# Optimization experiments

Hardware: AMD Instinct MI355X
Metric: run time of the kernel (lower is better)

Reference implementation:

```python
import jax, jax.numpy as jnp
import numpy as np
import math

B, S, D, H = 2, 2048, 1024, 16
HD = D // H  # head dim = 64


def _rope_tables():
    # RoFormer sinusoidal position embedding: one frequency per (even, odd) pair
    pos = jnp.arange(S, dtype=jnp.float32)[:, None]                # [S, 1]
    inv_freq = 1.0 / (10000.0 ** (jnp.arange(0, HD, 2, dtype=jnp.float32) / HD))  # [HD/2]
    ang = pos * inv_freq[None, :]                                   # [S, HD/2]
    sin = jnp.sin(ang)[None, None]                                  # [1,1,S,HD/2]
    cos = jnp.cos(ang)[None, None]
    return sin, cos


def setup_inputs() -> dict:
    key = jax.random.key(0)
    k0, k1, k2, k3 = jax.random.split(key, 4)
    scale = 1.0 / math.sqrt(D)
    sin, cos = _rope_tables()
    return {
        "hidden_states": jax.random.normal(k0, (B, S, D), dtype=jnp.float32),
        "Wq": jax.random.normal(k1, (D, D), dtype=jnp.float32) * scale,
        "Wk": jax.random.normal(k2, (D, D), dtype=jnp.float32) * scale,
        "Wv": jax.random.normal(k3, (D, D), dtype=jnp.float32) * scale,
        "sin": sin,
        "cos": cos,
    }


def _split_heads(x):
    # [B,S,D] -> [B,H,S,HD]
    b, s, _ = x.shape
    return x.reshape(b, s, H, HD).transpose(0, 2, 1, 3)


def _apply_rotary(x, sin, cos):
    # x: [B,H,S,HD]; sin/cos broadcast as [1,1,S,HD/2]
    x1 = x[..., 0::2]
    x2 = x[..., 1::2]
    out = jnp.stack([x1 * cos - x2 * sin, x2 * cos + x1 * sin], axis=-1)
    return out.reshape(x.shape)


def reference(hidden_states, Wq, Wk, Wv, sin, cos):
    q = _apply_rotary(_split_heads(hidden_states @ Wq), sin, cos)  # [B,H,S,HD]
    k = _apply_rotary(_split_heads(hidden_states @ Wk), sin, cos)
    v = _apply_rotary(_split_heads(hidden_states @ Wv), sin, cos)  # note: RoPE on V too, per source
    scores = jnp.einsum("bhqd,bhkd->bhqk", q, k) / math.sqrt(HD)   # [B,H,S,S]
    probs = jax.nn.softmax(scores, axis=-1)
    ctx = jnp.einsum("bhqk,bhkd->bhqd", probs, v)                   # [B,H,S,HD]
    return ctx.transpose(0, 2, 1, 3).reshape(hidden_states.shape[0], S, D)
```

## Files before the change

### kernel.cpp

```cpp
#include <hip/hip_runtime.h>

typedef unsigned short u16;
typedef unsigned short u16x8 __attribute__((ext_vector_type(8)));
typedef unsigned short u16x4 __attribute__((ext_vector_type(4)));
typedef __bf16 bf16x8_t __attribute__((ext_vector_type(8)));
typedef float floatx4 __attribute__((ext_vector_type(4)));

#define BATCH 2
#define S_LEN 2048
#define D_DIM 1024
#define NH    16
#define HD    64

__device__ __forceinline__ u16 f2b(float f) {
  union { float f; unsigned int i; } c; c.f = f;
  const unsigned int i = c.i;
  return (u16)((i + 0x7FFFu + ((i >> 16) & 1u)) >> 16);
}
__device__ __forceinline__ bf16x8_t asbf(u16x8 v) {
  union { u16x8 u; bf16x8_t b; } c; c.u = v; return c.b;
}
__device__ __forceinline__ void load_lds16(const u16* g, u16* l) {
  __builtin_amdgcn_global_load_lds(
      (const __attribute__((address_space(1))) void*)g,
      (__attribute__((address_space(3))) void*)l, 16, 0, 0);
}

__device__ __attribute__((aligned(256))) u16 g_xb[(size_t)BATCH * S_LEN * D_DIM];
__device__ __attribute__((aligned(256))) u16 g_wt[3u * D_DIM * D_DIM];
__device__ __attribute__((aligned(256))) u16 g_qkv[3u * BATCH * S_LEN * D_DIM];

__global__ __launch_bounds__(256) void convert_x(const float* __restrict__ X) {
  const size_t i = ((size_t)blockIdx.x * 256 + threadIdx.x) * 8;
  floatx4 a = *(const floatx4*)(X + i);
  floatx4 b = *(const floatx4*)(X + i + 4);
  u16x8 o;
#pragma unroll
  for (int j = 0; j < 4; ++j) { o[j] = f2b(a[j]); o[4 + j] = f2b(b[j]); }
  *(u16x8*)(g_xb + i) = o;
}

__global__ __launch_bounds__(256) void transpose_w(const float* __restrict__ W, int z) {
  __shared__ u16 t[64][65];
  u16* Wt = g_wt + (size_t)z * D_DIM * D_DIM;
  const int k0 = blockIdx.x * 64;
  const int n0 = blockIdx.y * 64;
  const int tid = threadIdx.x;
  const int rr = tid >> 4;
  const int cc = (tid & 15) * 4;
#pragma unroll
  for (int i = 0; i < 4; ++i) {
    const int r = rr + i * 16;
    floatx4 v = *(const floatx4*)(W + (size_t)(k0 + r) * D_DIM + n0 + cc);
    t[r][cc] = f2b(v[0]); t[r][cc + 1] = f2b(v[1]);
    t[r][cc + 2] = f2b(v[2]); t[r][cc + 3] = f2b(v[3]);
  }
  __syncthreads();
#pragma unroll
  for (int i = 0; i < 4; ++i) {
    const int r = rr + i * 16;
    u16x4 v;
    v[0] = t[cc][r]; v[1] = t[cc + 1][r]; v[2] = t[cc + 2][r]; v[3] = t[cc + 3][r];
    *(u16x4*)(Wt + (size_t)(n0 + r) * D_DIM + k0 + cc) = v;
  }
}

__global__ __launch_bounds__(256) void qkv_gemm(const float* __restrict__ sin_t,
                                                const float* __restrict__ cos_t) {
  __shared__ __attribute__((aligned(16))) u16 lds_a[128 * 32];
  __shared__ __attribute__((aligned(16))) u16 lds_b[128 * 32];
  const int tid = threadIdx.x;
  const int wv = tid >> 6;
  const int lane = tid & 63;
  const int lrow = lane & 15;
  const int quad = lane >> 4;
  const int wr = wv >> 1, wc = wv & 1;
  const int m0 = blockIdx.x * 128;
  const int n0 = blockIdx.y * 128;
  const int z = blockIdx.z;
  const bool vmode = (z == 2);
  const u16* Wz = g_wt + (size_t)z * (D_DIM * D_DIM);

  floatx4 acc[4][4] = {};

  const int srow = lane >> 2;
  const int scol = (lane & 3) * 8;
  const u16* gA = g_xb + (size_t)(m0 + wv * 32 + srow) * D_DIM + scol;
  const u16* gB = Wz   + (size_t)(n0 + wv * 32 + srow) * D_DIM + scol;
  u16* sA = &lds_a[(wv * 32) * 32];
  u16* sB = &lds_b[(wv * 32) * 32];

  const u16* Aarr = vmode ? lds_b : lds_a;
  const u16* Barr = vmode ? lds_a : lds_b;

  for (int k0 = 0; k0 < D_DIM; k0 += 32) {
    __syncthreads();
    load_lds16(gA + k0, sA);
    load_lds16(gA + (size_t)16 * D_DIM + k0, sA + 512);
    load_lds16(gB + k0, sB);
    load_lds16(gB + (size_t)16 * D_DIM + k0, sB + 512);
    __syncthreads();
    u16x8 af[4], bfr[4];
#pragma unroll
    for (int mi = 0; mi < 4; ++mi)
      af[mi] = *(const u16x8*)&Aarr[(wr * 64 + mi * 16 + lrow) * 32 + quad * 8];
#pragma unroll
    for (int ni = 0; ni < 4; ++ni)
      bfr[ni] = *(const u16x8*)&Barr[(wc * 64 + ni * 16 + lrow) * 32 + quad * 8];
#pragma unroll
    for (int mi = 0; mi < 4; ++mi)
#pragma unroll
      for (int ni = 0; ni < 4; ++ni)
        acc[mi][ni] = __builtin_amdgcn_mfma_f32_16x16x32_bf16(
            asbf(af[mi]), asbf(bfr[ni]), acc[mi][ni], 0, 0, 0);
  }

  if (!vmode) {
    u16* outz = g_qkv + (size_t)z * (BATCH * S_LEN * D_DIM);
#pragma unroll
    for (int mi = 0; mi < 4; ++mi) {
      const int m = m0 + wr * 64 + mi * 16 + quad * 4;
      const int b = m >> 11;
#pragma unroll
      for (int ni = 0; ni < 4; ++ni) {
        const int n = n0 + wc * 64 + ni * 16 + lrow;
        const int h = n >> 6, hd = n & 63;
        const int i0 = hd >> 1;
        const float sgn = (hd & 1) ? 1.f : -1.f;
        u16* op = outz + (((size_t)(b * NH + h) * S_LEN + (m & 2047)) * HD + hd);
#pragma unroll
        for (int r = 0; r < 4; ++r) {
          const int s = (m + r) & 2047;
          const float c  = cos_t[(size_t)s * 32 + i0];
          const float sn = sin_t[(size_t)s * 32 + i0];
          const float v = acc[mi][ni][r];
          const float vp = __shfl_xor(v, 1);
          op[r * HD] = f2b(v * c + sgn * sn * vp);
        }
      }
    }
  } else {
    u16* outv = g_qkv + (size_t)2 * (BATCH * S_LEN * D_DIM);
#pragma unroll
    for (int mi = 0; mi < 4; ++mi) {
      const int hb = n0 + wr * 64 + mi * 16 + quad * 4;
#pragma unroll
      for (int ni = 0; ni < 4; ++ni) {
        const int sg = m0 + wc * 64 + ni * 16 + lrow;
        const int b = sg >> 11, s = sg & 2047;
#pragma unroll
        for (int r = 0; r < 4; ++r) {
          const int hdg = hb + r;
          const int h = (hdg >> 6) & 15, hd = hdg & 63;
          const float c  = cos_t[(size_t)s * 32 + (hd >> 1)];
          const float sn = sin_t[(size_t)s * 32 + (hd >> 1)];
          const float v  = acc[mi][ni][r];
          const float vp = acc[mi][ni][r ^ 1];
          const float val = (r & 1) ? (v * c + sn * vp) : (v * c - sn * vp);
          outv[((size_t)(b * NH + h) * HD + hd) * S_LEN + s] = f2b(val);
        }
      }
    }
  }
}

__global__ __launch_bounds__(256) void flash_attn(float* __restrict__ out) {
  __shared__ __attribute__((aligned(16))) u16 lds_k[64 * 72];
  __shared__ __attribute__((aligned(16))) u16 lds_v[64 * 72];
  __shared__ __attribute__((aligned(16))) u16 lds_p[4][16 * 64];
  const int bh = blockIdx.x;
  const int qt = blockIdx.y;
  const int b = bh >> 4, h = bh & 15;
  const int tid = threadIdx.x, wv = tid >> 6, lane = tid & 63;
  const int lrow = lane & 15, quad = lane >> 4;
  const u16* Qb  = g_qkv + (size_t)bh * (S_LEN * HD);
  const u16* Kb  = g_qkv + (size_t)(BATCH * NH + bh) * (S_LEN * HD);
  const u16* VTb = g_qkv + (size_t)(2 * BATCH * NH + bh) * (S_LEN * HD);
  const int q0 = qt * 64 + wv * 16;

  u16x8 qf[2];
#pragma unroll
  for (int ks = 0; ks < 2; ++ks)
    qf[ks] = *(const u16x8*)(Qb + (size_t)(q0 + lrow) * HD + ks * 32 + quad * 8);

  floatx4 oacc[4] = {};
  float l_part[4] = {0.f, 0.f, 0.f, 0.f};
  const float cexp = 0.125f * 1.44269504088896f;

  const int sr = tid >> 3;
  const int sc = (tid & 7) * 8;
  u16* lp = lds_p[wv];

  for (int t = 0; t < S_LEN / 64; ++t) {
    const int kv0 = t * 64;
#pragma unroll
    for (int i = 0; i < 2; ++i) {
      const int r = sr + i * 32;
      *(u16x8*)&lds_k[r * 72 + sc] =
          *(const u16x8*)(Kb + (size_t)(kv0 + r) * HD + sc);
      *(u16x8*)&lds_v[r * 72 + sc] =
          *(const u16x8*)(VTb + (size_t)r * S_LEN + kv0 + sc);
    }
    __syncthreads();

    floatx4 sacc[4] = {};
#pragma unroll
    for (int nb = 0; nb < 4; ++nb)
#pragma unroll
      for (int ks = 0; ks < 2; ++ks) {
        u16x8 kf = *(const u16x8*)&lds_k[(nb * 16 + lrow) * 72 + ks * 32 + quad * 8];
        sacc[nb] = __builtin_amdgcn_mfma_f32_16x16x32_bf16(
            asbf(qf[ks]), asbf(kf), sacc[nb], 0, 0, 0);
      }

#pragma unroll
    for (int nb = 0; nb < 4; ++nb) {
      const int kvhi = 2 * nb + (lrow >> 3);
#pragma unroll
      for (int r = 0; r < 4; ++r) {
        const float p = exp2f(sacc[nb][r] * cexp);
        l_part[r] += p;
        const int q = quad * 4 + r;
        const int key = (kvhi ^ (q & 7) ^ ((q >> 3) << 1)) & 7;
        lp[q * 64 + key * 8 + (lrow & 7)] = f2b(p);
      }
    }

#pragma unroll
    for (int ks = 0; ks < 2; ++ks) {
      const int keyp = ((ks * 4 + quad) ^ (lrow & 7) ^ ((lrow >> 3) << 1)) & 7;
      u16x8 pf = *(const u16x8*)&lp[lrow * 64 + keyp * 8];
#pragma unroll
      for (int hb = 0; hb < 4; ++hb) {
        u16x8 vf = *(const u16x8*)&lds_v[(hb * 16 + lrow) * 72 + ks * 32 + quad * 8];
        oacc[hb] = __builtin_amdgcn_mfma_f32_16x16x32_bf16(
            asbf(pf), asbf(vf), oacc[hb], 0, 0, 0);
      }
    }
    __syncthreads();
  }

  float l_i[4];
#pragma unroll
  for (int r = 0; r < 4; ++r) {
    float l = l_part[r];
#pragma unroll
    for (int d = 1; d < 16; d <<= 1) l += __shfl_xor(l, d);
    l_i[r] = l;
  }

#pragma unroll
  for (int hb = 0; hb < 4; ++hb) {
    const int hd = hb * 16 + lrow;
#pragma unroll
    for (int r = 0; r < 4; ++r) {
      const int q = q0 + quad * 4 + r;
      out[((size_t)(b * S_LEN) + q) * D_DIM + h * HD + hd] = oacc[hb][r] / l_i[r];
    }
  }
}

extern "C" void kernel_launch(void* const* d_in, const int* in_sizes, int n_in,
                              void* d_out, int out_size, void* d_ws, size_t ws_size,
                              hipStream_t stream) {
  const float* X = (const float*)d_in[0];
  const float* sin_t = (const float*)d_in[4];
  const float* cos_t = (const float*)d_in[5];

  convert_x<<<2048, 256, 0, stream>>>(X);

  for (int z = 0; z < 3; ++z)
    transpose_w<<<dim3(16, 16), 256, 0, stream>>>((const float*)d_in[1 + z], z);

  qkv_gemm<<<dim3(32, 8, 3), 256, 0, stream>>>(sin_t, cos_t);

  flash_attn<<<dim3(32, 32), 256, 0, stream>>>((float*)d_out);
}
```

Baseline: 222.4 us.

## Merge prep kernels and swap MFMA operands to pack P stores

The separate x-conversion and three weight-transpose launches become one prep kernel with a 4-slice grid, cutting launch overhead. In flash attention the QK^T MFMA operands are swapped so each lane holds four consecutive keys for one query. P can then be packed into bf16 pairs with byte_perm and written as one 8-byte LDS store into a padded layout instead of swizzled scalar stores. The row-sum reduction shrinks to two shuffles plus broadcasts, and the final divide becomes a reciprocal multiply. P rounding changes from round-to-nearest to truncation, which adds a little numerical error.

Result: faster. 212.7 us (-4.4%).

```diff
diff --git a/kernel.cpp b/kernel.cpp
--- a/kernel.cpp
+++ b/kernel.cpp
@@ -17,6 +17,9 @@
   const unsigned int i = c.i;
   return (u16)((i + 0x7FFFu + ((i >> 16) & 1u)) >> 16);
 }
+__device__ __forceinline__ unsigned int fbits(float f) {
+  union { float f; unsigned int i; } c; c.f = f; return c.i;
+}
 __device__ __forceinline__ bf16x8_t asbf(u16x8 v) {
   union { u16x8 u; bf16x8_t b; } c; c.u = v; return c.b;
 }
@@ -30,22 +33,30 @@
 __device__ __attribute__((aligned(256))) u16 g_wt[3u * D_DIM * D_DIM];
 __device__ __attribute__((aligned(256))) u16 g_qkv[3u * BATCH * S_LEN * D_DIM];
 
-__global__ __launch_bounds__(256) void convert_x(const float* __restrict__ X) {
-  const size_t i = ((size_t)blockIdx.x * 256 + threadIdx.x) * 8;
-  floatx4 a = *(const floatx4*)(X + i);
-  floatx4 b = *(const floatx4*)(X + i + 4);
-  u16x8 o;
-#pragma unroll
-  for (int j = 0; j < 4; ++j) { o[j] = f2b(a[j]); o[4 + j] = f2b(b[j]); }
-  *(u16x8*)(g_xb + i) = o;
-}
-
-__global__ __launch_bounds__(256) void transpose_w(const float* __restrict__ W, int z) {
+__global__ __launch_bounds__(256) void prep(const float* __restrict__ X,
+                                            const float* __restrict__ Wq,
+                                            const float* __restrict__ Wk,
+                                            const float* __restrict__ Wv) {
+  const int tid = threadIdx.x;
+  const int z = blockIdx.y;
+  if (z == 3) {
+#pragma unroll
+    for (int c = 0; c < 8; ++c) {
+      const size_t i = (((size_t)c * 256 + blockIdx.x) * 256 + tid) * 8;
+      floatx4 a = *(const floatx4*)(X + i);
+      floatx4 b = *(const floatx4*)(X + i + 4);
+      u16x8 o;
+#pragma unroll
+      for (int j = 0; j < 4; ++j) { o[j] = f2b(a[j]); o[4 + j] = f2b(b[j]); }
+      *(u16x8*)(g_xb + i) = o;
+    }
+    return;
+  }
   __shared__ u16 t[64][65];
+  const float* W = (z == 0) ? Wq : (z == 1) ? Wk : Wv;
   u16* Wt = g_wt + (size_t)z * D_DIM * D_DIM;
-  const int k0 = blockIdx.x * 64;
-  const int n0 = blockIdx.y * 64;
-  const int tid = threadIdx.x;
+  const int k0 = (blockIdx.x & 15) * 64;
+  const int n0 = (blockIdx.x >> 4) * 64;
   const int rr = tid >> 4;
   const int cc = (tid & 15) * 4;
 #pragma unroll
@@ -167,7 +178,7 @@
 __global__ __launch_bounds__(256) void flash_attn(float* __restrict__ out) {
   __shared__ __attribute__((aligned(16))) u16 lds_k[64 * 72];
   __shared__ __attribute__((aligned(16))) u16 lds_v[64 * 72];
-  __shared__ __attribute__((aligned(16))) u16 lds_p[4][16 * 64];
+  __shared__ __attribute__((aligned(16))) u16 lds_p[4][16 * 72];
   const int bh = blockIdx.x;
   const int qt = blockIdx.y;
   const int b = bh >> 4, h = bh & 15;
@@ -184,7 +195,7 @@
     qf[ks] = *(const u16x8*)(Qb + (size_t)(q0 + lrow) * HD + ks * 32 + quad * 8);
 
   floatx4 oacc[4] = {};
-  float l_part[4] = {0.f, 0.f, 0.f, 0.f};
+  float l_part = 0.f;
   const float cexp = 0.125f * 1.44269504088896f;
 
   const int sr = tid >> 3;
@@ -210,26 +221,25 @@
       for (int ks = 0; ks < 2; ++ks) {
         u16x8 kf = *(const u16x8*)&lds_k[(nb * 16 + lrow) * 72 + ks * 32 + quad * 8];
         sacc[nb] = __builtin_amdgcn_mfma_f32_16x16x32_bf16(
-            asbf(qf[ks]), asbf(kf), sacc[nb], 0, 0, 0);
+            asbf(kf), asbf(qf[ks]), sacc[nb], 0, 0, 0);
       }
 
 #pragma unroll
     for (int nb = 0; nb < 4; ++nb) {
-      const int kvhi = 2 * nb + (lrow >> 3);
-#pragma unroll
-      for (int r = 0; r < 4; ++r) {
-        const float p = exp2f(sacc[nb][r] * cexp);
-        l_part[r] += p;
-        const int q = quad * 4 + r;
-        const int key = (kvhi ^ (q & 7) ^ ((q >> 3) << 1)) & 7;
-        lp[q * 64 + key * 8 + (lrow & 7)] = f2b(p);
-      }
+      float p0 = exp2f(sacc[nb][0] * cexp);
+      float p1 = exp2f(sacc[nb][1] * cexp);
+      float p2 = exp2f(sacc[nb][2] * cexp);
+      float p3 = exp2f(sacc[nb][3] * cexp);
+      l_part += (p0 + p1) + (p2 + p3);
+      uint2 pk;
+      pk.x = __byte_perm(fbits(p0), fbits(p1), 0x7632);
+      pk.y = __byte_perm(fbits(p2), fbits(p3), 0x7632);
+      *(uint2*)&lp[lrow * 72 + nb * 16 + quad * 4] = pk;
     }
 
 #pragma unroll
     for (int ks = 0; ks < 2; ++ks) {
-      const int keyp = ((ks * 4 + quad) ^ (lrow & 7) ^ ((lrow >> 3) << 1)) & 7;
-      u16x8 pf = *(const u16x8*)&lp[lrow * 64 + keyp * 8];
+      u16x8 pf = *(const u16x8*)&lp[lrow * 72 + ks * 32 + quad * 8];
 #pragma unroll
       for (int hb = 0; hb < 4; ++hb) {
         u16x8 vf = *(const u16x8*)&lds_v[(hb * 16 + lrow) * 72 + ks * 32 + quad * 8];
@@ -240,14 +250,13 @@
     __syncthreads();
   }
 
-  float l_i[4];
-#pragma unroll
-  for (int r = 0; r < 4; ++r) {
-    float l = l_part[r];
-#pragma unroll
-    for (int d = 1; d < 16; d <<= 1) l += __shfl_xor(l, d);
-    l_i[r] = l;
-  }
+  float l = l_part;
+  l += __shfl_xor(l, 16);
+  l += __shfl_xor(l, 32);
+  float linv[4];
+#pragma unroll
+  for (int r = 0; r < 4; ++r)
+    linv[r] = 1.f / __shfl(l, quad * 4 + r);
 
 #pragma unroll
   for (int hb = 0; hb < 4; ++hb) {
@@ -255,7 +264,7 @@
 #pragma unroll
     for (int r = 0; r < 4; ++r) {
       const int q = q0 + quad * 4 + r;
-      out[((size_t)(b * S_LEN) + q) * D_DIM + h * HD + hd] = oacc[hb][r] / l_i[r];
+      out[((size_t)(b * S_LEN) + q) * D_DIM + h * HD + hd] = oacc[hb][r] * linv[r];
     }
   }
 }
@@ -267,10 +276,9 @@
   const float* sin_t = (const float*)d_in[4];
   const float* cos_t = (const float*)d_in[5];
 
-  convert_x<<<2048, 256, 0, stream>>>(X);
-
-  for (int z = 0; z < 3; ++z)
-    transpose_w<<<dim3(16, 16), 256, 0, stream>>>((const float*)d_in[1 + z], z);
+  prep<<<dim3(256, 4), 256, 0, stream>>>(X, (const float*)d_in[1],
+                                         (const float*)d_in[2],
+                                         (const float*)d_in[3]);
 
   qkv_gemm<<<dim3(32, 8, 3), 256, 0, stream>>>(sin_t, cos_t);
 
```
